# Kernel optimization log

Hardware: AMD Instinct MI355X
Metric: run time of the kernel (lower is better)

The kernel has to match this reference:

```python
import jax, jax.numpy as jnp
import numpy as np
import math

N = 50000   # nodes
E = 800000  # edges
D = 128     # in/out dim
T = 4       # node types
H = 8       # heads (forced: Linear(8,64).view(-1, H, 8))
DK = D // H
HD = 8      # h_mat feature dim


def setup_inputs() -> dict:
    key = jax.random.key(0)
    ks = jax.random.split(key, 16)
    g = lambda k, shp, fan: jax.random.uniform(k, shp, jnp.float32, -1.0, 1.0) * math.sqrt(6.0 / fan)
    return {
        "meta_xs": jax.random.normal(ks[0], (N, D), jnp.float32),
        "node_type": jax.random.randint(ks[1], (N,), 0, T),
        "edge_index": jax.random.randint(ks[2], (2, E), 0, N),
        "h_mat": jax.random.normal(ks[3], (N, HD), jnp.float32),
        "sub_W": g(ks[4], (T, D, D), 2 * D),
        "sub_b": jnp.zeros((T, D), jnp.float32),
        "neigh_W": g(ks[5], (T, D, D), 2 * D),
        "neigh_b": jnp.zeros((T, D), jnp.float32),
        "hsub_W": g(ks[6], (HD, H * HD), HD + H * HD),
        "hsub_b": jnp.zeros((H * HD,), jnp.float32),
        "hneigh_W": g(ks[7], (HD, H * HD), HD + H * HD),
        "hneigh_b": jnp.zeros((H * HD,), jnp.float32),
        "relation_att": g(ks[8], (T, H, DK), H + DK),
        "relation_h_att": g(ks[9], (T, H, HD), H + HD),
        "ln_gamma": jnp.ones((D,), jnp.float32),
        "ln_beta": jnp.zeros((D,), jnp.float32),
    }


def _hgt_forward(meta_xs, h_mat, sub_W, sub_b, neigh_W, neigh_b, hsub_W, hsub_b,
                 hneigh_W, hneigh_b, relation_att, relation_h_att, ln_gamma, ln_beta,
                 node_type, edge_index):
    n = meta_xs.shape[0]
    e = edge_index.shape[1]
    src = edge_index[0]  # edge_index_j (neighbor)
    dst = edge_index[1]  # edge_index_i (sub / target)
    sqrt_dk = math.sqrt(DK)
    d_h = math.sqrt(H)

    # per-node, type-selected linear projections (sub by own type, neigh by own type)
    q_all = jnp.einsum('nd,tdo->tno', meta_xs, sub_W) + sub_b[:, None, :]      # [T,N,D]
    k_all = jnp.einsum('nd,tdo->tno', meta_xs, neigh_W) + neigh_b[:, None, :]  # [T,N,D]
    ar = jnp.arange(n)
    q_node = q_all[node_type, ar]  # [N,D] sub_linear[type_i](x_i)
    k_node = k_all[node_type, ar]  # [N,D] neigh_linear[type_j](x_j)

    h_sub_node = (h_mat @ hsub_W + hsub_b).reshape(n, H, HD)
    h_neigh_node = (h_mat @ hneigh_W + hneigh_b).reshape(n, H, HD)

    st = node_type[dst]  # sub type per edge selects relation params
    h_s = h_sub_node[dst]    # [E,H,8]
    h_n = h_neigh_node[src]  # [E,H,8]
    att_h = jnp.sum(jnp.tanh(h_s * h_n) * relation_h_att[st], axis=-1) / d_h  # [E,H]

    q_e = q_node[dst].reshape(e, H, DK)
    k_e = k_node[src].reshape(e, H, DK)
    att = jnp.sum(jnp.tanh(q_e * k_e) * relation_att[st], axis=-1) / sqrt_dk * att_h  # [E,H]

    # edge softmax over destination segments
    m = jax.ops.segment_max(att, dst, num_segments=n)  # [N,H]
    ea = jnp.exp(att - m[dst])
    denom = jax.ops.segment_sum(ea, dst, num_segments=n)
    alpha = ea / (denom[dst] + 1e-16)  # [E,H]

    msg = (k_e * alpha[:, :, None]).reshape(e, D)
    aggr = jax.ops.segment_sum(msg, dst, num_segments=n)  # [N,D]

    out = jax.nn.gelu(aggr, approximate=False)
    mu = jnp.mean(out, axis=-1, keepdims=True)
    var = jnp.var(out, axis=-1, keepdims=True)
    return (out - mu) * jax.lax.rsqrt(var + 1e-5) * ln_gamma + ln_beta


def reference(meta_xs, node_type, edge_index, h_mat, sub_W, sub_b, neigh_W, neigh_b,
              hsub_W, hsub_b, hneigh_W, hneigh_b, relation_att, relation_h_att,
              ln_gamma, ln_beta):
    return _hgt_forward(meta_xs, h_mat, sub_W, sub_b, neigh_W, neigh_b, hsub_W, hsub_b,
                        hneigh_W, hneigh_b, relation_att, relation_h_att, ln_gamma, ln_beta,
                        node_type, edge_index)
```

## Files before the change

### kernel.cpp

```cpp
#include <hip/hip_runtime.h>

typedef __bf16 bf16x8 __attribute__((ext_vector_type(8)));
typedef float f32x4 __attribute__((ext_vector_type(4)));

#define B_CHUNK 64
#define R_RANGE 2

__device__ __forceinline__ float exp2_fast(float x){
#if __has_builtin(__builtin_amdgcn_exp2f)
  return __builtin_amdgcn_exp2f(x);
#else
  return __expf(x * 0.69314718055994531f);
#endif
}
template<int CTRL>
__device__ __forceinline__ float dpp_add(float x){
  union { float f; int i; } a, b;
  a.f = x;
  b.i = __builtin_amdgcn_update_dpp(0, a.i, CTRL, 0xF, 0xF, true);
  return x + b.f;
}
__device__ __forceinline__ float sum4(float x){
  x = dpp_add<0xB1>(x);
  x = dpp_add<0x4E>(x);
  return x;
}
__device__ __forceinline__ unsigned int cvt_pk_bf16(float lo, float hi){
  unsigned int r;
  asm("v_cvt_pk_bf16_f32 %0, %1, %2" : "=v"(r) : "v"(lo), "v"(hi));
  return r;
}
__device__ __forceinline__ unsigned short f2bf1(float f){
  return (unsigned short)cvt_pk_bf16(f, f);
}
__device__ __forceinline__ bf16x8 ld_bf8(const unsigned short* p){
  union { uint4 u; bf16x8 v; } c;
  c.u = *reinterpret_cast<const uint4*>(p);
  return c.v;
}
__device__ __forceinline__ bf16x8 ld_f32_to_bf8(const float* p){
  float4 lo = *reinterpret_cast<const float4*>(p);
  float4 hi = *reinterpret_cast<const float4*>(p + 4);
  union { unsigned int u[4]; bf16x8 v; } c;
  c.u[0] = cvt_pk_bf16(lo.x, lo.y);
  c.u[1] = cvt_pk_bf16(lo.z, lo.w);
  c.u[2] = cvt_pk_bf16(hi.x, hi.y);
  c.u[3] = cvt_pk_bf16(hi.z, hi.w);
  return c.v;
}

__global__ __launch_bounds__(256) void k_prep(const int* ntype, int* tcur, int* nbt,
                       int Npad, int N,
                       const float* subW, const float* neighW,
                       unsigned short* wts, unsigned short* wtn,
                       const int* ei, int E, unsigned short* hist,
                       unsigned short* rank, int RNG, int HR, int NB){
  __shared__ unsigned int lsh[12544];
  int b = blockIdx.x;
  const int SB1 = B_CHUNK * R_RANGE;
  if (b < SB1){
    int cb = b & (B_CHUNK - 1);
    int r  = b >> 6;
    int lo = r * RNG;
    int bins = RNG >> 1;
    for (int i = threadIdx.x; i < bins; i += 256) lsh[i] = 0;
    __syncthreads();
    int C = (E + B_CHUNK - 1) / B_CHUNK;
    int e0 = cb * C;
    int e1 = e0 + C; if (e1 > E) e1 = E;
    for (int i = e0 + threadIdx.x; i < e1; i += 256){
      int d = ei[E + i] - lo;
      if ((unsigned)d < (unsigned)RNG){
        unsigned old = atomicAdd(&lsh[d >> 1], (d & 1) ? 65536u : 1u);
        rank[i] = (unsigned short)((old >> ((d & 1) << 4)) & 0xffffu);
      }
    }
    __syncthreads();
    unsigned int* hrow = reinterpret_cast<unsigned int*>(hist + (size_t)cb*HR + lo);
    for (int i = threadIdx.x; i < bins; i += 256) hrow[i] = lsh[i];
  } else if (b < SB1 + NB){
    int i = (b - SB1)*256 + threadIdx.x;
    if (i >= N) return;
    int lane = threadIdx.x & 63;
    int myt = ntype[i];
    unsigned long long below = (lane == 0) ? 0ull : ((~0ull) >> (64 - lane));
    #pragma unroll
    for (int tt = 0; tt < 4; ++tt){
      unsigned long long mask = __ballot(myt == tt);
      if (mask){
        int leader = __ffsll((long long)mask) - 1;
        int base = 0;
        if (lane == leader) base = atomicAdd(&tcur[tt], __popcll(mask));
        base = __shfl(base, leader);
        if (myt == tt){
          int pos = base + __popcll(mask & below);
          nbt[tt*Npad + pos] = i;
        }
      }
    }
  } else {
    int i = (b - SB1 - NB)*256 + threadIdx.x;
    int w = i >> 16;
    int r = i & 65535;
    int t = r >> 14;
    int rem = r & 16383;
    int o = rem >> 7;
    int kd = rem & 127;
    const float* src = w ? neighW : subW;
    unsigned short* dstp = w ? wtn : wts;
    dstp[(t << 14) + (o << 7) + kd] = f2bf1(src[(t << 14) + (kd << 7) + o]);
  }
}

__global__ __launch_bounds__(256) void k_mid(unsigned short* hist, int HR,
                       int* deg, int N, int SCB,
                       const float* h_mat, const float* hsW, const float* hsb,
                       const float* hnW, const float* hnb,
                       float2* hs2, char* hnc, unsigned short* bucket){
  int b = blockIdx.x;
  if (b < SCB){
    int d = b*256 + threadIdx.x;
    if (d >= N) return;
    unsigned run = 0;
    #pragma unroll 4
    for (int c = 0; c < B_CHUNK; ++c){
      unsigned short* p = hist + (size_t)c*HR + d;
      unsigned v = *p;
      *p = (unsigned short)run;
      run += v;
    }
    deg[d] = (int)run;
    if (run < 128) bucket[(size_t)d*128 + run] = 0;
  } else {
    int i = (b - SCB)*256 + threadIdx.x;
    if (i >= N*32) return;
    int n = i >> 5, l = i & 31;
    const float* hm = h_mat + (size_t)n*8;
    const float2* hsW2 = reinterpret_cast<const float2*>(hsW);
    const float2* hnW2 = reinterpret_cast<const float2*>(hnW);
    float s0=0.f, s1=0.f, n0=0.f, n1=0.f;
    #pragma unroll
    for (int d = 0; d < 8; ++d){
      float hv = hm[d];
      float2 ws2 = hsW2[d*32 + l];
      float2 wn2 = hnW2[d*32 + l];
      s0 += hv * ws2.x; s1 += hv * ws2.y;
      n0 += hv * wn2.x; n1 += hv * wn2.y;
    }
    float2 bs = reinterpret_cast<const float2*>(hsb)[l];
    float2 bn = reinterpret_cast<const float2*>(hnb)[l];
    hs2[(size_t)i] = make_float2(s0 + bs.x, s1 + bs.y);
    *reinterpret_cast<unsigned int*>(hnc + (size_t)n*128 + l*4)
        = cvt_pk_bf16(n0 + bn.x, n1 + bn.y);
  }
}

__global__ __launch_bounds__(256) void k_ms(const float* X,
      const unsigned short* wts, const unsigned short* wtn,
      const float* sub_b, const float* neigh_b,
      const int* nbt, const int* tcur, int Npad,
      float* q, char* kkc,
      const int* ei, unsigned short* bucket, int E,
      const unsigned short* hist, int HR, const unsigned short* rank, int MB){
  int b = blockIdx.x;
  if (b < MB){
    int t = -1, chunk = 0, acc = 0;
    #pragma unroll
    for (int tt = 0; tt < 4; ++tt){
      int cnt = tcur[tt];
      int nc = (cnt + 63) >> 6;
      if (t < 0 && b < acc + nc){ t = tt; chunk = b - acc; }
      acc += nc;
    }
    if (t < 0) return;
    int lane = threadIdx.x & 63;
    int w = threadIdx.x >> 6;
    int quad = lane >> 4, l16 = lane & 15;
    int cnt = tcur[t];
    int p = chunk*64 + w*16 + l16;
    bool ok = p < cnt;
    int nid = nbt[t*Npad + (ok ? p : 0)];
    bf16x8 xb[4];
    #pragma unroll
    for (int kk = 0; kk < 4; ++kk)
      xb[kk] = ld_f32_to_bf8(X + (size_t)nid*128 + kk*32 + quad*8);
    #pragma unroll
    for (int pj = 0; pj < 2; ++pj){
      const unsigned short* Wt = pj ? wtn : wts;
      const float* bias = pj ? neigh_b : sub_b;
      #pragma unroll
      for (int ot = 0; ot < 8; ++ot){
        f32x4 c = {0.f, 0.f, 0.f, 0.f};
        #pragma unroll
        for (int kk = 0; kk < 4; ++kk){
          bf16x8 wa = ld_bf8(Wt + ((size_t)t << 14) + ((size_t)(ot*16 + l16) << 7)
                                + kk*32 + quad*8);
          c = __builtin_amdgcn_mfma_f32_16x16x32_bf16(wa, xb[kk], c, 0, 0, 0);
        }
        int o0 = ot*16 + quad*4;
        float4 b4 = *reinterpret_cast<const float4*>(bias + t*128 + o0);
        if (ok){
          if (pj == 0){
            float4 v = make_float4(c[0]+b4.x, c[1]+b4.y, c[2]+b4.z, c[3]+b4.w);
            *reinterpret_cast<float4*>(q + (size_t)nid*128 + o0) = v;
          } else {
            uint2 pk;
            pk.x = cvt_pk_bf16(c[0]+b4.x, c[1]+b4.y);
            pk.y = cvt_pk_bf16(c[2]+b4.z, c[3]+b4.w);
            *reinterpret_cast<uint2*>(kkc + ((size_t)nid << 8) + (size_t)(o0 << 1)) = pk;
          }
        }
      }
    }
  } else {
    int sb = b - MB;
    int cb = sb >> 3;
    int sub = sb & 7;
    int C = (E + B_CHUNK - 1) / B_CHUNK;
    int seg = (C + 7) >> 3;
    int s0 = sub*seg;
    int s1 = s0 + seg; if (s1 > C) s1 = C;
    int e0 = cb*C + s0;
    int e1 = cb*C + s1; if (e1 > E) e1 = E;
    const unsigned short* hrow = hist + (size_t)cb*HR;
    for (int i = e0 + threadIdx.x; i < e1; i += 256){
      int d = ei[E + i];
      int pos = (int)hrow[d] + (int)rank[i];
      if (pos < 128) bucket[(size_t)d*128 + pos] = (unsigned short)ei[i];
    }
  }
}

__global__ __launch_bounds__(256) void k_edge(const float* q, const char* kkc,
      const char* hnc, const float2* hs2, const int* degA,
      const unsigned short* bucket, const int* ntype,
      const float* rel_att, const float* rel_h_att,
      const float* ln_g, const float* ln_b,
      float* out, int n0, int n1){
  int wid = n0 + ((blockIdx.x*blockDim.x + threadIdx.x) >> 6);
  if (wid >= n1) return;
  int lane = threadIdx.x & 63;
  int l = lane & 31;
  int half = (lane >> 5) & 1;
  int t4 = l & 3, head = l >> 2;
  const float TLOG2E = 2.8853900817779268f;
  float4 qv = *reinterpret_cast<const float4*>(q + (size_t)wid*128 + l*4);
  float qe0 = qv.x*TLOG2E, qe1 = qv.y*TLOG2E, qe2 = qv.z*TLOG2E, qe3 = qv.w*TLOG2E;
  float2 hv = hs2[(size_t)wid*32 + l];
  float he0 = hv.x*TLOG2E, he1 = hv.y*TLOG2E;
  int st = ntype[wid];
  int rb = st*8 + head;
  float4 ra = *reinterpret_cast<const float4*>(rel_att + rb*16 + t4*4);
  float2 rh = *reinterpret_cast<const float2*>(rel_h_att + rb*8 + t4*2);
  float c0 = -0.5f*ra.x, c1 = -0.5f*ra.y, c2 = -0.5f*ra.z, c3 = -0.5f*ra.w;
  float cs = 0.25f*(ra.x + ra.y + ra.z + ra.w);
  const float HSC = 0.35355339059327373f * 1.4426950408889634f;
  float rh0 = rh.x*HSC, rh1 = rh.y*HSC;
  float ch0 = -2.f*rh0, ch1 = -2.f*rh1, chs = rh0 + rh1;
  float s = 0.f, a0 = 0.f, a1 = 0.f, a2 = 0.f, a3 = 0.f;

  int deg = __builtin_amdgcn_readfirstlane(degA[wid]);
  if (deg > 128) deg = 128;
  unsigned bkt = reinterpret_cast<const unsigned*>(bucket)[(size_t)wid*64 + lane];
  int niter = (deg + 1) >> 1;
  int glim = (deg + 1 - half) >> 1;
  const char* kk_l = kkc + l*8;
  const char* hn_l = hnc + l*4;

  struct KH { uint2 k; unsigned h; };
  auto lp = [&](int g)->KH {
    int gg = g < niter ? g : 0;
    unsigned v = (unsigned)__builtin_amdgcn_readlane((int)bkt, gg);
    int sy = half ? (int)(v >> 16) : (int)(v & 0xffffu);
    KH r;
    r.k = *reinterpret_cast<const uint2*>(kk_l + ((size_t)(unsigned)sy << 8));
    r.h = *reinterpret_cast<const unsigned*>(hn_l + ((size_t)(unsigned)sy << 7));
    return r;
  };
  auto pr = [&](KH P, int g){
    union { unsigned u; float f; } k0,k1,k2,k3,h0,h1;
    k0.u = P.k.x << 16; k1.u = P.k.x & 0xffff0000u;
    k2.u = P.k.y << 16; k3.u = P.k.y & 0xffff0000u;
    h0.u = P.h << 16;   h1.u = P.h & 0xffff0000u;
    float e0 = exp2_fast(qe0*k0.f), e1 = exp2_fast(qe1*k1.f);
    float e2 = exp2_fast(qe2*k2.f), e3 = exp2_fast(qe3*k3.f);
    float f0 = exp2_fast(he0*h0.f), f1 = exp2_fast(he1*h1.f);
    float d0 = e0 + 1.f, d1 = e1 + 1.f, d2 = e2 + 1.f, d3 = e3 + 1.f;
    float dh0 = f0 + 1.f, dh1 = f1 + 1.f;
    float R01 = __builtin_amdgcn_rcpf(d0*d1);
    float R23 = __builtin_amdgcn_rcpf(d2*d3);
    float Rh  = __builtin_amdgcn_rcpf(dh0*dh1);
    float r0 = d1*R01, r1 = d0*R01;
    float r2 = d3*R23, r3 = d2*R23;
    float g0 = dh1*Rh, g1 = dh0*Rh;
    float pp = fmaf(c0,r0, fmaf(c1,r1, fmaf(c2,r2, fmaf(c3,r3, cs))));
    float ph = fmaf(ch0,g0, fmaf(ch1,g1, chs));
    pp = sum4(pp);
    ph = sum4(ph);
    float w = exp2_fast(pp * ph);
    w = (g < glim) ? w : 0.f;
    s += w;
    a0 = fmaf(w, k0.f, a0); a1 = fmaf(w, k1.f, a1);
    a2 = fmaf(w, k2.f, a2); a3 = fmaf(w, k3.f, a3);
  };

  if (niter > 0){
    KH A = lp(0);
    KH B = lp(1);
    for (int g = 0; g < niter; g += 2){
      KH C = lp(g+2);
      pr(A, g);
      KH D = lp(g+3);
      if (g+1 < niter) pr(B, g+1);
      A = C; B = D;
    }
  }
  s  += __shfl_xor(s, 32);
  a0 += __shfl_xor(a0, 32); a1 += __shfl_xor(a1, 32);
  a2 += __shfl_xor(a2, 32); a3 += __shfl_xor(a3, 32);

  float inv = 1.0f / (s + 1e-16f);
  float x0 = a0*inv, x1 = a1*inv, x2 = a2*inv, x3 = a3*inv;
  const float IS2 = 0.70710678118654752f;
  x0 = 0.5f*x0*(1.f + erff(x0*IS2));
  x1 = 0.5f*x1*(1.f + erff(x1*IS2));
  x2 = 0.5f*x2*(1.f + erff(x2*IS2));
  x3 = 0.5f*x3*(1.f + erff(x3*IS2));
  float sm = x0+x1+x2+x3;
  float sq = x0*x0 + x1*x1 + x2*x2 + x3*x3;
  #pragma unroll
  for (int d = 1; d < 32; d <<= 1){ sm += __shfl_xor(sm, d); sq += __shfl_xor(sq, d); }
  float mu = sm * (1.f/128.f);
  float var = fmaxf(sq * (1.f/128.f) - mu*mu, 0.f);
  float r = rsqrtf(var + 1e-5f);
  if (half == 0){
    float4 g4 = *reinterpret_cast<const float4*>(ln_g + l*4);
    float4 b4 = *reinterpret_cast<const float4*>(ln_b + l*4);
    float4 o4 = make_float4((x0-mu)*r*g4.x + b4.x, (x1-mu)*r*g4.y + b4.y,
                            (x2-mu)*r*g4.z + b4.z, (x3-mu)*r*g4.w + b4.w);
    *reinterpret_cast<float4*>(out + (size_t)wid*128 + l*4) = o4;
  }
}

extern "C" void kernel_launch(void* const* d_in, const int* in_sizes, int n_in,
                              void* d_out, int out_size, void* d_ws, size_t ws_size,
                              hipStream_t stream) {
  const float* meta_xs  = (const float*)d_in[0];
  const int*   node_type= (const int*)d_in[1];
  const int*   edge_idx = (const int*)d_in[2];
  const float* h_mat    = (const float*)d_in[3];
  const float* sub_W    = (const float*)d_in[4];
  const float* sub_b    = (const float*)d_in[5];
  const float* neigh_W  = (const float*)d_in[6];
  const float* neigh_b  = (const float*)d_in[7];
  const float* hsub_W   = (const float*)d_in[8];
  const float* hsub_b   = (const float*)d_in[9];
  const float* hneigh_W = (const float*)d_in[10];
  const float* hneigh_b = (const float*)d_in[11];
  const float* rel_att  = (const float*)d_in[12];
  const float* rel_hatt = (const float*)d_in[13];
  const float* ln_g     = (const float*)d_in[14];
  const float* ln_b     = (const float*)d_in[15];

  const int N = in_sizes[0] / 128;
  const int E = in_sizes[2] / 2;
  const int Npad = (N + 63) & ~63;
  const int RNG = (((N + R_RANGE - 1) / R_RANGE) + 1) & ~1;
  const int HR  = RNG * R_RANGE;

  char* wbase = (char*)d_ws;
  size_t o = 0;
  auto carve = [&](size_t bytes)->char* {
    char* p = wbase + o;
    o = (o + bytes + 255) & ~(size_t)255;
    return p;
  };
  float*          q      = (float*)carve((size_t)N*128*4);
  char*           kkc    = carve((size_t)N*256);
  char*           hnc    = carve((size_t)N*128);
  float2*         hs2    = (float2*)carve((size_t)N*32*8);
  unsigned short* bucket = (unsigned short*)carve((size_t)N*128*2);
  unsigned short* hist   = (unsigned short*)carve((size_t)B_CHUNK*HR*2);
  unsigned short* rank   = (unsigned short*)carve((size_t)E*2);
  int*            deg    = (int*)carve((size_t)N*4);
  int*            tmeta  = (int*)carve(64);
  int*            nbt    = (int*)carve((size_t)4*Npad*4);
  unsigned short* wts    = (unsigned short*)carve((size_t)4*128*128*2);
  unsigned short* wtn    = (unsigned short*)carve((size_t)4*128*128*2);
  if (o > ws_size) return;

  int* tcur = tmeta;

  const int SB1 = B_CHUNK * R_RANGE;
  const int NB  = (N + 255) / 256;
  const int WB  = (2*4*128*128) / 256;
  const int SCB = (N + 255) / 256;
  const int HB  = (N*32 + 255) / 256;
  const int MB  = ((N + 63) >> 6) + 4;
  const int SB3 = B_CHUNK * 8;

  hipMemsetAsync(tmeta, 0, 64, stream);
  k_prep <<<SB1 + NB + WB, 256, 0, stream>>>(node_type, tcur, nbt, Npad, N,
                                       sub_W, neigh_W, wts, wtn,
                                       edge_idx, E, hist, rank, RNG, HR, NB);
  k_mid  <<<SCB + HB, 256, 0, stream>>>(hist, HR, deg, N, SCB,
                                       h_mat, hsub_W, hsub_b, hneigh_W, hneigh_b,
                                       hs2, hnc, bucket);
  k_ms   <<<MB + SB3, 256, 0, stream>>>(meta_xs, wts, wtn, sub_b, neigh_b,
                                       nbt, tcur, Npad, q, kkc,
                                       edge_idx, bucket, E, hist, HR, rank, MB);
  const int Nh = N >> 1;
  k_edge <<<(Nh+3)/4, 256, 0, stream>>>(q, kkc, hnc, hs2, deg, bucket, node_type,
                                       rel_att, rel_hatt, ln_g, ln_b,
                                       (float*)d_out, 0, Nh);
  k_edge <<<((N-Nh)+3)/4, 256, 0, stream>>>(q, kkc, hnc, hs2, deg, bucket, node_type,
                                       rel_att, rel_hatt, ln_g, ln_b,
                                       (float*)d_out, Nh, N);
}
```

Before: 294.1 us.

## Replace per-node histogram bucketing with two-level radix partition of edges

Swaps the fine-grained per-destination histogram, rank and scatter scheme for a two-level radix sort. Edges are first coarse-binned by the destination's high bits into fixed-capacity segments, using per-chunk counts, a cross-chunk scan and an LDS-staged scatter. A new k_fin kernel then finely sorts each segment in shared memory and writes the per-node buckets and degrees. The aim is to drop the large 16-bit histogram and rank arrays and make the global scatters coalesced, at the cost of an extra kernel launch, large LDS use in k_ms that may cut occupancy of the MFMA blocks, and silent truncation if a coarse segment exceeds its fixed capacity.

```diff
diff --git a/kernel.cpp b/kernel.cpp
--- a/kernel.cpp
+++ b/kernel.cpp
@@ -3,8 +3,10 @@
 typedef __bf16 bf16x8 __attribute__((ext_vector_type(8)));
 typedef float f32x4 __attribute__((ext_vector_type(4)));
 
-#define B_CHUNK 64
-#define R_RANGE 2
+#define CBC   128
+#define CEMAX 6272
+#define CAP   6144
+#define NRSH  8
 
 __device__ __forceinline__ float exp2_fast(float x){
 #if __has_builtin(__builtin_amdgcn_exp2f)
@@ -48,40 +50,36 @@
   c.u[3] = cvt_pk_bf16(hi.z, hi.w);
   return c.v;
 }
-
-__global__ __launch_bounds__(256) void k_prep(const int* ntype, int* tcur, int* nbt,
-                       int Npad, int N,
+__device__ __forceinline__ unsigned wave_excl(unsigned x, int lane, unsigned* total){
+  unsigned inc = x;
+  #pragma unroll
+  for (int off = 1; off < 64; off <<= 1){
+    unsigned t = (unsigned)__shfl_up((int)inc, off);
+    if (lane >= off) inc += t;
+  }
+  *total = (unsigned)__shfl((int)inc, 63);
+  return inc - x;
+}
+
+__global__ __launch_bounds__(256) void k_prep(const int* ei, int E, int CE, int NR,
+                       unsigned* cnt,
+                       const int* ntype, int* tcur, int* nbt, int Npad, int N,
                        const float* subW, const float* neighW,
-                       unsigned short* wts, unsigned short* wtn,
-                       const int* ei, int E, unsigned short* hist,
-                       unsigned short* rank, int RNG, int HR, int NB){
-  __shared__ unsigned int lsh[12544];
-  int b = blockIdx.x;
-  const int SB1 = B_CHUNK * R_RANGE;
-  if (b < SB1){
-    int cb = b & (B_CHUNK - 1);
-    int r  = b >> 6;
-    int lo = r * RNG;
-    int bins = RNG >> 1;
-    for (int i = threadIdx.x; i < bins; i += 256) lsh[i] = 0;
-    __syncthreads();
-    int C = (E + B_CHUNK - 1) / B_CHUNK;
-    int e0 = cb * C;
-    int e1 = e0 + C; if (e1 > E) e1 = E;
-    for (int i = e0 + threadIdx.x; i < e1; i += 256){
-      int d = ei[E + i] - lo;
-      if ((unsigned)d < (unsigned)RNG){
-        unsigned old = atomicAdd(&lsh[d >> 1], (d & 1) ? 65536u : 1u);
-        rank[i] = (unsigned short)((old >> ((d & 1) << 4)) & 0xffffu);
-      }
-    }
-    __syncthreads();
-    unsigned int* hrow = reinterpret_cast<unsigned int*>(hist + (size_t)cb*HR + lo);
-    for (int i = threadIdx.x; i < bins; i += 256) hrow[i] = lsh[i];
-  } else if (b < SB1 + NB){
-    int i = (b - SB1)*256 + threadIdx.x;
+                       unsigned short* wts, unsigned short* wtn, int NB){
+  __shared__ unsigned h[256];
+  int b = blockIdx.x, tid = threadIdx.x;
+  if (b < CBC){
+    h[tid] = 0;
+    __syncthreads();
+    int e0 = b*CE, e1 = e0 + CE; if (e1 > E) e1 = E;
+    for (int i = e0 + tid; i < e1; i += 256)
+      atomicAdd(&h[(unsigned)ei[E + i] >> NRSH], 1u);
+    __syncthreads();
+    if (tid < NR) cnt[(size_t)b*NR + tid] = h[tid];
+  } else if (b < CBC + NB){
+    int i = (b - CBC)*256 + tid;
     if (i >= N) return;
-    int lane = threadIdx.x & 63;
+    int lane = tid & 63;
     int myt = ntype[i];
     unsigned long long below = (lane == 0) ? 0ull : ((~0ull) >> (64 - lane));
     #pragma unroll
@@ -99,7 +97,7 @@
       }
     }
   } else {
-    int i = (b - SB1 - NB)*256 + threadIdx.x;
+    int i = (b - CBC - NB)*256 + tid;
     int w = i >> 16;
     int r = i & 65535;
     int t = r >> 14;
@@ -112,27 +110,25 @@
   }
 }
 
-__global__ __launch_bounds__(256) void k_mid(unsigned short* hist, int HR,
-                       int* deg, int N, int SCB,
+__global__ __launch_bounds__(256) void k_scan(const unsigned* cnt, unsigned* cbase,
+                       unsigned* rtot, int NR,
                        const float* h_mat, const float* hsW, const float* hsb,
                        const float* hnW, const float* hnb,
-                       float2* hs2, char* hnc, unsigned short* bucket){
-  int b = blockIdx.x;
-  if (b < SCB){
-    int d = b*256 + threadIdx.x;
-    if (d >= N) return;
-    unsigned run = 0;
-    #pragma unroll 4
-    for (int c = 0; c < B_CHUNK; ++c){
-      unsigned short* p = hist + (size_t)c*HR + d;
-      unsigned v = *p;
-      *p = (unsigned short)run;
-      run += v;
-    }
-    deg[d] = (int)run;
-    if (run < 128) bucket[(size_t)d*128 + run] = 0;
+                       float2* hs2, char* hnc, int N){
+  int b = blockIdx.x, tid = threadIdx.x;
+  if (b < NR){
+    if (tid < 64){
+      int r = b;
+      unsigned v0 = cnt[(size_t)(2*tid)*NR + r];
+      unsigned v1 = cnt[(size_t)(2*tid + 1)*NR + r];
+      unsigned tot;
+      unsigned ex = wave_excl(v0 + v1, tid, &tot);
+      cbase[(size_t)(2*tid)*NR + r]     = (unsigned)r*CAP + ex;
+      cbase[(size_t)(2*tid + 1)*NR + r] = (unsigned)r*CAP + ex + v0;
+      if (tid == 0) rtot[r] = tot;
+    }
   } else {
-    int i = (b - SCB)*256 + threadIdx.x;
+    int i = (b - NR)*256 + tid;
     if (i >= N*32) return;
     int n = i >> 5, l = i & 31;
     const float* hm = h_mat + (size_t)n*8;
@@ -160,25 +156,30 @@
       const float* sub_b, const float* neigh_b,
       const int* nbt, const int* tcur, int Npad,
       float* q, char* kkc,
-      const int* ei, unsigned short* bucket, int E,
-      const unsigned short* hist, int HR, const unsigned short* rank, int MB){
-  int b = blockIdx.x;
+      const int* ei, int E, int CE, int NR,
+      const unsigned* cbase, unsigned* coarse, int MB){
+  __shared__ unsigned lb[256];
+  __shared__ unsigned cur[256];
+  __shared__ int      fb[256];
+  __shared__ unsigned stage[CEMAX];
+  __shared__ unsigned char rid[CEMAX];
+  int b = blockIdx.x, tid = threadIdx.x;
   if (b < MB){
     int t = -1, chunk = 0, acc = 0;
     #pragma unroll
     for (int tt = 0; tt < 4; ++tt){
-      int cnt = tcur[tt];
-      int nc = (cnt + 63) >> 6;
+      int cntn = tcur[tt];
+      int nc = (cntn + 63) >> 6;
       if (t < 0 && b < acc + nc){ t = tt; chunk = b - acc; }
       acc += nc;
     }
     if (t < 0) return;
-    int lane = threadIdx.x & 63;
-    int w = threadIdx.x >> 6;
+    int lane = tid & 63;
+    int w = tid >> 6;
     int quad = lane >> 4, l16 = lane & 15;
-    int cnt = tcur[t];
+    int cntn = tcur[t];
     int p = chunk*64 + w*16 + l16;
-    bool ok = p < cnt;
+    bool ok = p < cntn;
     int nid = nbt[t*Npad + (ok ? p : 0)];
     bf16x8 xb[4];
     #pragma unroll
@@ -213,21 +214,87 @@
       }
     }
   } else {
-    int sb = b - MB;
-    int cb = sb >> 3;
-    int sub = sb & 7;
-    int C = (E + B_CHUNK - 1) / B_CHUNK;
-    int seg = (C + 7) >> 3;
-    int s0 = sub*seg;
-    int s1 = s0 + seg; if (s1 > C) s1 = C;
-    int e0 = cb*C + s0;
-    int e1 = cb*C + s1; if (e1 > E) e1 = E;
-    const unsigned short* hrow = hist + (size_t)cb*HR;
-    for (int i = e0 + threadIdx.x; i < e1; i += 256){
+    int cb = b - MB;
+    lb[tid] = 0;
+    __syncthreads();
+    int e0 = cb*CE, e1 = e0 + CE; if (e1 > E) e1 = E;
+    for (int i = e0 + tid; i < e1; i += 256)
+      atomicAdd(&lb[(unsigned)ei[E + i] >> NRSH], 1u);
+    __syncthreads();
+    if (tid < 64){
+      unsigned a0=lb[4*tid], a1=lb[4*tid+1], a2=lb[4*tid+2], a3=lb[4*tid+3];
+      unsigned tot;
+      unsigned ex = wave_excl(a0+a1+a2+a3, tid, &tot);
+      lb[4*tid]=ex; lb[4*tid+1]=ex+a0; lb[4*tid+2]=ex+a0+a1; lb[4*tid+3]=ex+a0+a1+a2;
+    }
+    __syncthreads();
+    cur[tid] = lb[tid];
+    if (tid < NR) fb[tid] = (int)cbase[(size_t)cb*NR + tid] - (int)lb[tid];
+    __syncthreads();
+    for (int i = e0 + tid; i < e1; i += 256){
       int d = ei[E + i];
-      int pos = (int)hrow[d] + (int)rank[i];
-      if (pos < 128) bucket[(size_t)d*128 + pos] = (unsigned short)ei[i];
-    }
+      unsigned r = (unsigned)d >> NRSH;
+      unsigned slot = atomicAdd(&cur[r], 1u);
+      stage[slot] = ((unsigned)(d & ((1 << NRSH) - 1)) << 16)
+                  | ((unsigned)ei[i] & 0xffffu);
+      rid[slot] = (unsigned char)r;
+    }
+    __syncthreads();
+    int m = e1 - e0;
+    for (int s = tid; s < m; s += 256){
+      unsigned r = rid[s];
+      unsigned pos = (unsigned)(fb[r] + s);
+      if (pos < (r + 1)*(unsigned)CAP) coarse[pos] = stage[s];
+    }
+  }
+}
+
+__global__ __launch_bounds__(256) void k_fin(const unsigned* coarse,
+                       const unsigned* rtot, int N,
+                       unsigned short* bucket, int* deg){
+  __shared__ unsigned dh[257];
+  __shared__ unsigned dcur[256];
+  __shared__ unsigned short sorted[CAP];
+  __shared__ unsigned char ldst[CAP];
+  int r = blockIdx.x, tid = threadIdx.x;
+  unsigned m = rtot[r]; if (m > (unsigned)CAP) m = CAP;
+  dh[tid] = 0;
+  if (tid == 0) dh[256] = 0;
+  __syncthreads();
+  const unsigned* seg = coarse + (size_t)r*CAP;
+  for (unsigned i = tid; i < m; i += 256) atomicAdd(&dh[seg[i] >> 16], 1u);
+  __syncthreads();
+  if (tid < 64){
+    unsigned a0=dh[4*tid], a1=dh[4*tid+1], a2=dh[4*tid+2], a3=dh[4*tid+3];
+    unsigned tot;
+    unsigned ex = wave_excl(a0+a1+a2+a3, tid, &tot);
+    dh[4*tid]=ex; dh[4*tid+1]=ex+a0; dh[4*tid+2]=ex+a0+a1; dh[4*tid+3]=ex+a0+a1+a2;
+    if (tid == 0) dh[256] = tot;
+  }
+  __syncthreads();
+  dcur[tid] = dh[tid];
+  __syncthreads();
+  for (unsigned i = tid; i < m; i += 256){
+    unsigned e = seg[i];
+    unsigned dl = e >> 16;
+    unsigned p = atomicAdd(&dcur[dl], 1u);
+    sorted[p] = (unsigned short)(e & 0xffffu);
+    ldst[p] = (unsigned char)dl;
+  }
+  __syncthreads();
+  for (unsigned i = tid; i < m; i += 256){
+    unsigned dl = ldst[i];
+    unsigned off = i - dh[dl];
+    if (off < 128u){
+      int d = (r << NRSH) + (int)dl;
+      bucket[(size_t)d*128 + off] = sorted[i];
+    }
+  }
+  int d = (r << NRSH) + tid;
+  if (d < N){
+    unsigned c = dh[tid + 1] - dh[tid];
+    deg[d] = (int)c;
+    if (c < 128u) bucket[(size_t)d*128 + c] = 0;
   }
 }
 
@@ -365,8 +432,8 @@
   const int N = in_sizes[0] / 128;
   const int E = in_sizes[2] / 2;
   const int Npad = (N + 63) & ~63;
-  const int RNG = (((N + R_RANGE - 1) / R_RANGE) + 1) & ~1;
-  const int HR  = RNG * R_RANGE;
+  const int NR = (N + (1 << NRSH) - 1) >> NRSH;
+  const int CE = (E + CBC - 1) / CBC;
 
   char* wbase = (char*)d_ws;
   size_t o = 0;
@@ -380,8 +447,10 @@
   char*           hnc    = carve((size_t)N*128);
   float2*         hs2    = (float2*)carve((size_t)N*32*8);
   unsigned short* bucket = (unsigned short*)carve((size_t)N*128*2);
-  unsigned short* hist   = (unsigned short*)carve((size_t)B_CHUNK*HR*2);
-  unsigned short* rank   = (unsigned short*)carve((size_t)E*2);
+  unsigned*       cnt    = (unsigned*)carve((size_t)CBC*NR*4);
+  unsigned*       cbase  = (unsigned*)carve((size_t)CBC*NR*4);
+  unsigned*       rtot   = (unsigned*)carve((size_t)NR*4);
+  unsigned*       coarse = (unsigned*)carve((size_t)NR*CAP*4);
   int*            deg    = (int*)carve((size_t)N*4);
   int*            tmeta  = (int*)carve(64);
   int*            nbt    = (int*)carve((size_t)4*Npad*4);
@@ -391,24 +460,22 @@
 
   int* tcur = tmeta;
 
-  const int SB1 = B_CHUNK * R_RANGE;
   const int NB  = (N + 255) / 256;
   const int WB  = (2*4*128*128) / 256;
-  const int SCB = (N + 255) / 256;
   const int HB  = (N*32 + 255) / 256;
   const int MB  = ((N + 63) >> 6) + 4;
-  const int SB3 = B_CHUNK * 8;
 
   hipMemsetAsync(tmeta, 0, 64, stream);
-  k_prep <<<SB1 + NB + WB, 256, 0, stream>>>(node_type, tcur, nbt, Npad, N,
-                                       sub_W, neigh_W, wts, wtn,
-                                       edge_idx, E, hist, rank, RNG, HR, NB);
-  k_mid  <<<SCB + HB, 256, 0, stream>>>(hist, HR, deg, N, SCB,
+  k_prep <<<CBC + NB + WB, 256, 0, stream>>>(edge_idx, E, CE, NR, cnt,
+                                       node_type, tcur, nbt, Npad, N,
+                                       sub_W, neigh_W, wts, wtn, NB);
+  k_scan <<<NR + HB, 256, 0, stream>>>(cnt, cbase, rtot, NR,
                                        h_mat, hsub_W, hsub_b, hneigh_W, hneigh_b,
-                                       hs2, hnc, bucket);
-  k_ms   <<<MB + SB3, 256, 0, stream>>>(meta_xs, wts, wtn, sub_b, neigh_b,
+                                       hs2, hnc, N);
+  k_ms   <<<MB + CBC, 256, 0, stream>>>(meta_xs, wts, wtn, sub_b, neigh_b,
                                        nbt, tcur, Npad, q, kkc,
-                                       edge_idx, bucket, E, hist, HR, rank, MB);
+                                       edge_idx, E, CE, NR, cbase, coarse, MB);
+  k_fin  <<<NR, 256, 0, stream>>>(coarse, rtot, N, bucket, deg);
   const int Nh = N >> 1;
   k_edge <<<(Nh+3)/4, 256, 0, stream>>>(q, kkc, hnc, hs2, deg, bucket, node_type,
                                        rel_att, rel_hatt, ln_g, ln_b,
```

Measured after the change: 284.4 us. 1.03x faster.
